# Kernel optimization log

Measured on AMD Instinct MI355X. Metric: run time of the kernel, lower is better.

Reference implementation:

```python
import jax, jax.numpy as jnp
import numpy as np

N = 100000      # nodes
E = 3200000     # edges
F_IN = 128      # input node features
G = 64          # graphs in batch
A = 32          # action_shape


def _fanin_uniform(key, shape):
    v = 1.0 / np.sqrt(shape[0])
    return jax.random.uniform(key, shape, jnp.float32, -v, v)


def setup_inputs() -> dict:
    key = jax.random.key(0)
    ks = jax.random.split(key, 16)
    x = jax.random.normal(ks[0], (N, F_IN), jnp.float32)
    edge_index = jax.random.randint(ks[1], (2, E), 0, N, jnp.int64)
    batch = jnp.sort(jax.random.randint(ks[2], (N,), 0, G, jnp.int64))
    init_w = 0.003
    return {
        "x": x,
        "edge_index": edge_index,
        "batch": batch,
        # GCN weights are [in, out] (old-style PyG GCNConv .weight)
        "W1": _fanin_uniform(ks[3], (F_IN, 16)), "b1": jnp.zeros((16,), jnp.float32),
        "W2": _fanin_uniform(ks[4], (16, 64)),   "b2": jnp.zeros((64,), jnp.float32),
        "W3": _fanin_uniform(ks[5], (64, 32)),   "b3": jnp.zeros((32,), jnp.float32),
        # MLP head (Linear stores [out, in]; we keep [in, out] and matmul directly)
        "Wa": _fanin_uniform(ks[6], (32, 64)),   "ba": jnp.zeros((64,), jnp.float32),
        "Wo": jax.random.uniform(ks[7], (64, A), jnp.float32, -init_w, init_w),
        "bo": jnp.zeros((A,), jnp.float32),
    }


def _gcn_conv(x, W, b, src, dst, dinv):
    # GCNConv: D^{-1/2}(A+I)D^{-1/2} X W + b, symmetric norm with self-loops.
    h = x @ W                                   # [N, out] small GEMM
    coef = dinv[src] * dinv[dst]                # [E]
    msg = h[src] * coef[:, None]                # gather + scale (memory-bound)
    agg = jax.ops.segment_sum(msg, dst, num_segments=N)  # scatter-add
    agg = agg + h * (dinv * dinv)[:, None]      # self-loop contribution
    return agg + b


def reference(x, edge_index, batch, W1, b1, W2, b2, W3, b3, Wa, ba, Wo, bo):
    src, dst = edge_index[0], edge_index[1]
    # degree with self-loops (edge weights = 1)
    deg = jax.ops.segment_sum(jnp.ones((E,), x.dtype), dst, num_segments=N) + 1.0
    dinv = jax.lax.rsqrt(deg)

    h = jax.nn.relu(_gcn_conv(x, W1, b1, src, dst, dinv))   # dropout: eval no-op
    h = jax.nn.relu(_gcn_conv(h, W2, b2, src, dst, dinv))
    h = _gcn_conv(h, W3, b3, src, dst, dinv)                # [N, 32]

    # global_mean_pool over batch ids
    sums = jax.ops.segment_sum(h, batch, num_segments=G)            # [G, 32]
    cnts = jax.ops.segment_sum(jnp.ones((N,), h.dtype), batch, num_segments=G)
    pooled = sums / jnp.maximum(cnts, 1.0)[:, None]

    a = jax.nn.relu(pooled @ Wa + ba)
    return jnp.tanh(a @ Wo + bo)                             # [G, A]
```

## Files before the change

### kernel.cpp

```cpp
#include <hip/hip_runtime.h>
#include <hip/hip_bf16.h>
#include <math.h>


#define THREADS 256
#define TCSR 512
#define BSH 8
#define MAXNB 512
#define CH_E 2048
#define CPT 8

typedef __attribute__((ext_vector_type(8))) short short8;
typedef __attribute__((ext_vector_type(4))) float f32x4;

__device__ inline unsigned short f2bf(float f) {
    unsigned int u = __float_as_uint(f);
    return (unsigned short)((u + 0x7fffu + ((u >> 16) & 1u)) >> 16);
}
__device__ inline unsigned int pk2bf(float a, float b) {
    return (unsigned int)f2bf(a) | ((unsigned int)f2bf(b) << 16);
}
__device__ inline float bflo(unsigned int u) { return __uint_as_float(u << 16); }
__device__ inline float bfhi(unsigned int u) { return __uint_as_float(u & 0xffff0000u); }
__device__ inline void unpk8(const uint4 u, float* f) {
    f[0] = bflo(u.x); f[1] = bfhi(u.x); f[2] = bflo(u.y); f[3] = bfhi(u.y);
    f[4] = bflo(u.z); f[5] = bfhi(u.z); f[6] = bflo(u.w); f[7] = bfhi(u.w);
}

__global__ void k_countA(const int* __restrict__ dst, unsigned short* __restrict__ lp16,
                         int* __restrict__ cnt_mat, int E, int NB, int NCH) {
    __shared__ int hist[MAXNB];
    int t = threadIdx.x, chunk = blockIdx.x;
    for (int h = t; h < NB; h += THREADS) hist[h] = 0;
    __syncthreads();
    int e0 = chunk * CH_E, e1 = min(E, e0 + CH_E);
    for (int e = e0 + t; e < e1; e += THREADS) {
        int h = dst[e] >> BSH;
        int lp = atomicAdd(&hist[h], 1);
        lp16[e] = (unsigned short)lp;
    }
    __syncthreads();
    for (int h = t; h < NB; h += THREADS) cnt_mat[(size_t)h * NCH + chunk] = hist[h];
}

__global__ void k_sumK1(const int* __restrict__ cnt_mat, int* __restrict__ bucket_tot, int NCH) {
    __shared__ int red[THREADS];
    int b = blockIdx.x, t = threadIdx.x;
    int s = 0;
    for (int c = t; c < NCH; c += THREADS) s += cnt_mat[(size_t)b * NCH + c];
    red[t] = s;
    __syncthreads();
    for (int off = THREADS / 2; off > 0; off >>= 1) {
        if (t < off) red[t] += red[t + off];
        __syncthreads();
    }
    if (t == 0) bucket_tot[b] = red[0];
}

__global__ void k_scanK2(const int* __restrict__ bucket_tot, int* __restrict__ bucket_base,
                         int* __restrict__ rowptr, int NB, int E, int N) {
    __shared__ int sh[MAXNB];
    int t = threadIdx.x;
    int v = (t < NB) ? bucket_tot[t] : 0;
    sh[t] = v;
    __syncthreads();
    for (int off = 1; off < MAXNB; off <<= 1) {
        int u = (t >= off) ? sh[t - off] : 0;
        __syncthreads();
        sh[t] += u;
        __syncthreads();
    }
    if (t < NB) bucket_base[t] = sh[t] - v;
    if (t == 0) { bucket_base[NB] = E; rowptr[N] = E; }
}

__global__ void k_scanK3(const int* __restrict__ cnt_mat, const int* __restrict__ bucket_base,
                         int* __restrict__ offs_mat, int NCH) {
    __shared__ int sh[THREADS];
    int b = blockIdx.x, t = threadIdx.x;
    int c0 = t * CPT;
    int v[CPT];
    int s = 0;
#pragma unroll
    for (int k = 0; k < CPT; ++k) {
        int c = c0 + k;
        v[k] = (c < NCH) ? cnt_mat[(size_t)b * NCH + c] : 0;
        s += v[k];
    }
    sh[t] = s;
    __syncthreads();
    for (int off = 1; off < THREADS; off <<= 1) {
        int u = (t >= off) ? sh[t - off] : 0;
        __syncthreads();
        sh[t] += u;
        __syncthreads();
    }
    int run = bucket_base[b] + sh[t] - s;
#pragma unroll
    for (int k = 0; k < CPT; ++k) {
        int c = c0 + k;
        if (c < NCH) { offs_mat[(size_t)b * NCH + c] = run; run += v[k]; }
    }
}

__global__ void k_scatter2(const int* __restrict__ src, const int* __restrict__ dst,
                           const unsigned short* __restrict__ lp16,
                           const int* __restrict__ offs_mat,
                           unsigned int* __restrict__ bedges, int E, int NB, int NCH) {
    __shared__ int offs[MAXNB];
    int t = threadIdx.x, chunk = blockIdx.x;
    for (int h = t; h < NB; h += THREADS) offs[h] = offs_mat[(size_t)h * NCH + chunk];
    __syncthreads();
    int e0 = chunk * CH_E, e1 = min(E, e0 + CH_E);
    for (int e = e0 + t; e < e1; e += THREADS) {
        int d = dst[e];
        int h = d >> BSH;
        int pos = offs[h] + (int)lp16[e];
        bedges[pos] = ((unsigned int)src[e] << BSH) | (unsigned int)(d & ((1 << BSH) - 1));
    }
}

__global__ void k_bucket_csr(const unsigned int* __restrict__ bedges,
                             const int* __restrict__ bucket_base,
                             int* __restrict__ rowptr, float* __restrict__ dinv,
                             int* __restrict__ csr_src, int N) {
    __shared__ int hist[256];
    __shared__ int sc[256];
    __shared__ int cur[256];
    int t = threadIdx.x;
    int b = blockIdx.x;
    int base = bucket_base[b];
    int end = bucket_base[b + 1];
    if (t < 256) hist[t] = 0;
    __syncthreads();
    for (int i = base + t; i < end; i += TCSR)
        atomicAdd(&hist[bedges[i] & 255], 1);
    __syncthreads();
    int c = 0;
    if (t < 256) { c = hist[t]; sc[t] = c; }
    __syncthreads();
    for (int off = 1; off < 256; off <<= 1) {
        int u = (t >= off && t < 256) ? sc[t - off] : 0;
        __syncthreads();
        if (t < 256) sc[t] += u;
        __syncthreads();
    }
    if (t < 256) {
        int excl = sc[t] - c;
        int node = (b << BSH) + t;
        if (node < N) {
            rowptr[node] = base + excl;
            dinv[node] = (float)(1.0 / sqrt((double)(c + 1)));
        }
        cur[t] = excl;
    }
    __syncthreads();
    for (int i = base + t; i < end; i += TCSR) {
        unsigned int u = bedges[i];
        int ln = (int)(u & 255);
        int p = atomicAdd(&cur[ln], 1);
        csr_src[base + p] = (int)(u >> BSH);
    }
}

__global__ __launch_bounds__(256) void k_gemm1(const float* __restrict__ X,
                        const float* __restrict__ W,
                        const float* __restrict__ dinv, unsigned short* __restrict__ H, int N) {
    __shared__ float Wt[16 * 128];
    int t = threadIdx.x;
    for (int i = t; i < 16 * 128; i += THREADS) {
        int j = i >> 7, k = i & 127;
        Wt[i] = W[k * 16 + j];
    }
    __syncthreads();
    int row = blockIdx.x * THREADS + t;
    if (row >= N) return;
    const float4* xr = (const float4*)(X + (size_t)row * 128);
    float acc[16];
#pragma unroll
    for (int j = 0; j < 16; ++j) acc[j] = 0.0f;
#pragma unroll 4
    for (int k4 = 0; k4 < 32; ++k4) {
        float4 xv = xr[k4];
#pragma unroll
        for (int j = 0; j < 16; ++j) {
            const float4 wv = *(const float4*)&Wt[j * 128 + k4 * 4];
            acc[j] += xv.x * wv.x + xv.y * wv.y + xv.z * wv.z + xv.w * wv.w;
        }
    }
    float di = dinv[row];
    uint4 oa, ob;
    oa.x = pk2bf(acc[0] * di, acc[1] * di);
    oa.y = pk2bf(acc[2] * di, acc[3] * di);
    oa.z = pk2bf(acc[4] * di, acc[5] * di);
    oa.w = pk2bf(acc[6] * di, acc[7] * di);
    ob.x = pk2bf(acc[8] * di, acc[9] * di);
    ob.y = pk2bf(acc[10] * di, acc[11] * di);
    ob.z = pk2bf(acc[12] * di, acc[13] * di);
    ob.w = pk2bf(acc[14] * di, acc[15] * di);
    uint4* outr = (uint4*)(H + (size_t)row * 16);
    outr[0] = oa;
    outr[1] = ob;
}

template<int F, int MODE, int S>
__global__ __launch_bounds__(256) void k_pull(
        const int* __restrict__ rowptr, const int* __restrict__ csr_src,
        const float* __restrict__ dinv, const unsigned short* __restrict__ Hb,
        const float* __restrict__ bias, void* __restrict__ outp,
        const int* __restrict__ batch, float* __restrict__ gsums,
        int N, int G) {
    const int LPN = F / 8;
    const int GRP = LPN * S;
    const int NPB = THREADS / GRP;
    int t = threadIdx.x;
    int idx = t % GRP;
    int fl = idx % LPN;
    int s  = idx / LPN;
    int fo = fl * 8;
    int node = blockIdx.x * NPB + t / GRP;

    float acc[8] = {0.f, 0.f, 0.f, 0.f, 0.f, 0.f, 0.f, 0.f};
    if (node < N) {
        int beg = rowptr[node], end = rowptr[node + 1];
        int i = beg + s;
        for (; i + 3 * S < end; i += 4 * S) {
            int s0 = csr_src[i];
            int s1 = csr_src[i + S];
            int s2 = csr_src[i + 2 * S];
            int s3 = csr_src[i + 3 * S];
            uint4 g0 = *(const uint4*)(Hb + (size_t)s0 * F + fo);
            uint4 g1 = *(const uint4*)(Hb + (size_t)s1 * F + fo);
            uint4 g2 = *(const uint4*)(Hb + (size_t)s2 * F + fo);
            uint4 g3 = *(const uint4*)(Hb + (size_t)s3 * F + fo);
            float f0[8], f1[8], f2[8], f3[8];
            unpk8(g0, f0); unpk8(g1, f1); unpk8(g2, f2); unpk8(g3, f3);
#pragma unroll
            for (int j = 0; j < 8; ++j) acc[j] += (f0[j] + f1[j]) + (f2[j] + f3[j]);
        }
        for (; i < end; i += S) {
            int sv = csr_src[i];
            uint4 g = *(const uint4*)(Hb + (size_t)sv * F + fo);
            float f[8];
            unpk8(g, f);
#pragma unroll
            for (int j = 0; j < 8; ++j) acc[j] += f[j];
        }
    }
#pragma unroll
    for (int j = 0; j < 8; ++j) {
        if (S >= 2) acc[j] += __shfl_xor(acc[j], LPN);
        if (S >= 4) acc[j] += __shfl_xor(acc[j], 2 * LPN);
    }

    if constexpr (MODE == 3) {
        __shared__ float lsum[4][32];
        __shared__ int g0s;
        for (int z = t; z < 4 * 32; z += THREADS) ((float*)lsum)[z] = 0.0f;
        if (t == 0) g0s = batch[blockIdx.x * NPB];
        __syncthreads();
        int g0 = g0s;
        if (node < N && s == 0) {
            uint4 gs = *(const uint4*)(Hb + (size_t)node * F + fo);
            float sf[8];
            unpk8(gs, sf);
            float di = dinv[node];
            int g = batch[node];
            int r = g - g0;
            if ((unsigned)r < 4u) {
#pragma unroll
                for (int j = 0; j < 8; ++j)
                    atomicAdd(&lsum[r][fo + j], di * (acc[j] + sf[j]));
            } else {
#pragma unroll
                for (int j = 0; j < 8; ++j)
                    atomicAdd(&gsums[(size_t)g * 32 + fo + j], di * (acc[j] + sf[j]));
            }
        }
        __syncthreads();
        if (t < 128) {
            int r = t >> 5, f = t & 31;
            int g = g0 + r;
            float v = lsum[r][f];
            if (g < G && v != 0.0f) atomicAdd(&gsums[(size_t)g * 32 + f], v);
        }
    } else {
        if (node < N && s == 0) {
            uint4 gs = *(const uint4*)(Hb + (size_t)node * F + fo);
            float sf[8];
            unpk8(gs, sf);
            float di = dinv[node];
            float tv[8];
#pragma unroll
            for (int j = 0; j < 8; ++j) tv[j] = di * (acc[j] + sf[j]);
            if constexpr (MODE == 1) {
                float w[8];
#pragma unroll
                for (int j = 0; j < 8; ++j) w[j] = fmaxf(tv[j] + bias[fo + j], 0.0f) * di;
                uint4 st;
                st.x = pk2bf(w[0], w[1]); st.y = pk2bf(w[2], w[3]);
                st.z = pk2bf(w[4], w[5]); st.w = pk2bf(w[6], w[7]);
                *(uint4*)((unsigned short*)outp + (size_t)node * F + fo) = st;
            } else {
                float* of = (float*)outp + (size_t)node * F + fo;
                float4 o0, o1;
                o0.x = tv[0]; o0.y = tv[1]; o0.z = tv[2]; o0.w = tv[3];
                o1.x = tv[4]; o1.y = tv[5]; o1.z = tv[6]; o1.w = tv[7];
                ((float4*)of)[0] = o0; ((float4*)of)[1] = o1;
            }
        }
    }
}

__global__ __launch_bounds__(256) void k_mlp(const float* __restrict__ P2,
                      const float* __restrict__ W2, const float* __restrict__ b2,
                      const float* __restrict__ W3, const float* __restrict__ dinv,
                      unsigned short* __restrict__ Hb3, int N) {
    __shared__ unsigned int aTd[4][32][17];
    int t = threadIdx.x;
    int w = t >> 6;
    int l = t & 63;
    int g = l >> 4;
    int c = l & 15;
    int node = blockIdx.x * 64 + w * 16 + c;
    bool nv = node < N;
    int cn = nv ? node : 0;

    short8 w2f[4];
#pragma unroll
    for (int mi = 0; mi < 4; ++mi) {
        short8 f = {0, 0, 0, 0, 0, 0, 0, 0};
        if (g < 2) {
            int j = 16 * mi + c;
#pragma unroll
            for (int e = 0; e < 8; ++e)
                f[e] = (short)f2bf(W2[(8 * g + e) * 64 + j]);
        }
        w2f[mi] = f;
    }
    short8 w3f[2][2];
#pragma unroll
    for (int mt = 0; mt < 2; ++mt)
#pragma unroll
        for (int kt = 0; kt < 2; ++kt) {
            short8 f;
#pragma unroll
            for (int e = 0; e < 8; ++e)
                f[e] = (short)f2bf(W3[(32 * kt + 8 * g + e) * 32 + 16 * mt + c]);
            w3f[mt][kt] = f;
        }
    float b2v[16];
#pragma unroll
    for (int mi = 0; mi < 4; ++mi)
#pragma unroll
        for (int r = 0; r < 4; ++r)
            b2v[4 * mi + r] = b2[16 * mi + 4 * g + r];

    short8 pf = {0, 0, 0, 0, 0, 0, 0, 0};
    if (g < 2) {
        const float4* pr = (const float4*)(P2 + (size_t)cn * 16 + 8 * g);
        float4 p0 = pr[0], p1 = pr[1];
        pf[0] = (short)f2bf(p0.x); pf[1] = (short)f2bf(p0.y);
        pf[2] = (short)f2bf(p0.z); pf[3] = (short)f2bf(p0.w);
        pf[4] = (short)f2bf(p1.x); pf[5] = (short)f2bf(p1.y);
        pf[6] = (short)f2bf(p1.z); pf[7] = (short)f2bf(p1.w);
    }

    f32x4 zero = {0.f, 0.f, 0.f, 0.f};
    f32x4 acc1[4];
#pragma unroll
    for (int mi = 0; mi < 4; ++mi)
        acc1[mi] = __builtin_amdgcn_mfma_f32_16x16x32_bf16(w2f[mi], pf, zero, 0, 0, 0);

#pragma unroll
    for (int mi = 0; mi < 4; ++mi) {
        float a0 = fmaxf(acc1[mi][0] + b2v[4 * mi + 0], 0.f);
        float a1 = fmaxf(acc1[mi][1] + b2v[4 * mi + 1], 0.f);
        float a2 = fmaxf(acc1[mi][2] + b2v[4 * mi + 2], 0.f);
        float a3 = fmaxf(acc1[mi][3] + b2v[4 * mi + 3], 0.f);
        aTd[w][8 * mi + 2 * g][c]     = pk2bf(a0, a1);
        aTd[w][8 * mi + 2 * g + 1][c] = pk2bf(a2, a3);
    }
    __syncthreads();

    short8 bfr[2];
#pragma unroll
    for (int kt = 0; kt < 2; ++kt) {
        short8 f;
#pragma unroll
        for (int i = 0; i < 4; ++i) {
            unsigned int d = aTd[w][16 * kt + 4 * g + i][c];
            f[2 * i]     = (short)(d & 0xffffu);
            f[2 * i + 1] = (short)(d >> 16);
        }
        bfr[kt] = f;
    }

    f32x4 acc2[2] = {{0.f, 0.f, 0.f, 0.f}, {0.f, 0.f, 0.f, 0.f}};
#pragma unroll
    for (int mt = 0; mt < 2; ++mt)
#pragma unroll
        for (int kt = 0; kt < 2; ++kt)
            acc2[mt] = __builtin_amdgcn_mfma_f32_16x16x32_bf16(w3f[mt][kt], bfr[kt], acc2[mt], 0, 0, 0);

    if (nv) {
        float di = dinv[node];
        unsigned short* o = Hb3 + (size_t)node * 32;
#pragma unroll
        for (int mt = 0; mt < 2; ++mt) {
            *(unsigned int*)(o + 16 * mt + 4 * g)     = pk2bf(acc2[mt][0] * di, acc2[mt][1] * di);
            *(unsigned int*)(o + 16 * mt + 4 * g + 2) = pk2bf(acc2[mt][2] * di, acc2[mt][3] * di);
        }
    }
}

__global__ void k_zero_f(float* p, int n) {
    int i = blockIdx.x * blockDim.x + threadIdx.x;
    if (i < n) p[i] = 0.0f;
}

__global__ void k_head(const float* __restrict__ sums, const int* __restrict__ batch, int N,
                       const float* __restrict__ b3,
                       const float* __restrict__ Wa, const float* __restrict__ ba,
                       const float* __restrict__ Wo, const float* __restrict__ bo,
                       float* __restrict__ out) {
    int g = blockIdx.x;
    int j = threadIdx.x;
    int lo = 0, hi = N;
    while (lo < hi) { int m = (lo + hi) >> 1; if (batch[m] < g) lo = m + 1; else hi = m; }
    int start = lo;
    lo = start; hi = N;
    while (lo < hi) { int m = (lo + hi) >> 1; if (batch[m] < g + 1) lo = m + 1; else hi = m; }
    int cnt = lo - start;
    float inv = 1.0f / (float)(cnt > 0 ? cnt : 1);

    __shared__ float p[32];
    __shared__ float a[64];
    if (j < 32) p[j] = sums[g * 32 + j] * inv + b3[j];
    __syncthreads();
    float acc = ba[j];
#pragma unroll
    for (int k = 0; k < 32; ++k) acc += p[k] * Wa[k * 64 + j];
    a[j] = fmaxf(acc, 0.0f);
    __syncthreads();
    if (j < 32) {
        float acc2 = bo[j];
#pragma unroll
        for (int k = 0; k < 64; ++k) acc2 += a[k] * Wo[k * 32 + j];
        out[g * 32 + j] = tanhf(acc2);
    }
}

static inline int cdiv(long long a, int b) { return (int)((a + b - 1) / b); }
static inline size_t align256(size_t x) { return (x + 255) & ~(size_t)255; }

extern "C" void kernel_launch(void* const* d_in, const int* in_sizes, int n_in,
                              void* d_out, int out_size, void* d_ws, size_t ws_size,
                              hipStream_t stream) {
    const float* x     = (const float*)d_in[0];
    const int*   edge  = (const int*)d_in[1];
    const int*   batch = (const int*)d_in[2];
    const float* W1 = (const float*)d_in[3];  const float* b1 = (const float*)d_in[4];
    const float* W2 = (const float*)d_in[5];  const float* b2 = (const float*)d_in[6];
    const float* W3 = (const float*)d_in[7];  const float* b3 = (const float*)d_in[8];
    const float* Wa = (const float*)d_in[9];  const float* ba = (const float*)d_in[10];
    const float* Wo = (const float*)d_in[11]; const float* bo = (const float*)d_in[12];

    const int E = in_sizes[1] / 2;
    const int N = in_sizes[2];
    const int G = 64;
    const int NB = cdiv(N, 1 << BSH);
    const int NCH = cdiv(E, CH_E);

    const int* srcp = edge;
    const int* dstp = edge + E;

    char* base = (char*)d_ws;
    size_t off = 0;
    float* dinv   = (float*)(base + off); off = align256(off + sizeof(float) * N);
    unsigned short* lp16 = (unsigned short*)(base + off); off = align256(off + sizeof(short) * E);
    int* cnt_mat  = (int*)(base + off); off = align256(off + sizeof(int) * (size_t)NB * NCH);
    int* offs_mat = (int*)(base + off); off = align256(off + sizeof(int) * (size_t)NB * NCH);
    int* btot     = (int*)(base + off); off = align256(off + sizeof(int) * (NB + 1));
    int* bbase    = (int*)(base + off); off = align256(off + sizeof(int) * (NB + 1));
    unsigned int* bedges = (unsigned int*)(base + off); off = align256(off + sizeof(int) * E);
    int* rowptr   = (int*)(base + off); off = align256(off + sizeof(int) * (N + 1));
    int* csr_src  = (int*)(base + off); off = align256(off + sizeof(int) * E);
    unsigned short* Hb1 = (unsigned short*)(base + off); off = align256(off + sizeof(short) * (size_t)N * 16);
    unsigned short* Hb2 = (unsigned short*)(base + off); off = align256(off + sizeof(short) * (size_t)N * 16);
    float* P2     = (float*)(base + off); off = align256(off + sizeof(float) * (size_t)N * 16);
    unsigned short* Hb3 = (unsigned short*)(base + off); off = align256(off + sizeof(short) * (size_t)N * 32);
    float* sums   = (float*)(base + off); off = align256(off + sizeof(float) * G * 32);

    k_countA<<<NCH, THREADS, 0, stream>>>(dstp, lp16, cnt_mat, E, NB, NCH);
    k_sumK1<<<NB, THREADS, 0, stream>>>(cnt_mat, btot, NCH);
    k_scanK2<<<1, MAXNB, 0, stream>>>(btot, bbase, rowptr, NB, E, N);
    k_scanK3<<<NB, THREADS, 0, stream>>>(cnt_mat, bbase, offs_mat, NCH);
    k_scatter2<<<NCH, THREADS, 0, stream>>>(srcp, dstp, lp16, offs_mat, bedges, E, NB, NCH);

    k_bucket_csr<<<NB, TCSR, 0, stream>>>(bedges, bbase, rowptr, dinv, csr_src, N);

    k_gemm1<<<cdiv(N, THREADS), THREADS, 0, stream>>>(x, W1, dinv, Hb1, N);
    k_pull<16, 1, 4><<<cdiv(N, 32), THREADS, 0, stream>>>(rowptr, csr_src, dinv, Hb1, b1, Hb2,
                                                          nullptr, nullptr, N, G);

    k_pull<16, 2, 4><<<cdiv(N, 32), THREADS, 0, stream>>>(rowptr, csr_src, dinv, Hb2, nullptr, P2,
                                                          nullptr, nullptr, N, G);

    k_mlp<<<cdiv(N, 64), THREADS, 0, stream>>>(P2, W2, b2, W3, dinv, Hb3, N);

    k_zero_f<<<cdiv(G * 32, THREADS), THREADS, 0, stream>>>(sums, G * 32);
    k_pull<32, 3, 2><<<cdiv(N, 32), THREADS, 0, stream>>>(rowptr, csr_src, dinv, Hb3, nullptr,
                                                          nullptr, batch, sums, N, G);

    k_head<<<G, 64, 0, stream>>>(sums, batch, N, b3, Wa, ba, Wo, bo, (float*)d_out);
}
```

Before: 310.5 us.

## Split layer-3 features into two 16-wide halves and pull each half separately

The layer-3 hidden state is stored as two separate 16-feature bf16 arrays instead of one 32-wide array, and the final aggregation-plus-pooling runs as a new kernel where each block handles one half for 64 nodes. Each half-array is 3.2 MB, so the random neighbour gathers touch a smaller footprint that fits better in cache. The cost is reading the CSR indices twice and issuing more global atomics into the pooled sums. The edge chunk size for CSR construction is also doubled.

```diff
diff --git a/kernel.cpp b/kernel.cpp
--- a/kernel.cpp
+++ b/kernel.cpp
@@ -7,7 +7,7 @@
 #define TCSR 512
 #define BSH 8
 #define MAXNB 512
-#define CH_E 2048
+#define CH_E 4096
 #define CPT 8
 
 typedef __attribute__((ext_vector_type(8))) short short8;
@@ -207,9 +207,7 @@
 __global__ __launch_bounds__(256) void k_pull(
         const int* __restrict__ rowptr, const int* __restrict__ csr_src,
         const float* __restrict__ dinv, const unsigned short* __restrict__ Hb,
-        const float* __restrict__ bias, void* __restrict__ outp,
-        const int* __restrict__ batch, float* __restrict__ gsums,
-        int N, int G) {
+        const float* __restrict__ bias, void* __restrict__ outp, int N) {
     const int LPN = F / 8;
     const int GRP = LPN * S;
     const int NPB = THREADS / GRP;
@@ -253,69 +251,118 @@
         if (S >= 4) acc[j] += __shfl_xor(acc[j], 2 * LPN);
     }
 
-    if constexpr (MODE == 3) {
-        __shared__ float lsum[4][32];
-        __shared__ int g0s;
-        for (int z = t; z < 4 * 32; z += THREADS) ((float*)lsum)[z] = 0.0f;
-        if (t == 0) g0s = batch[blockIdx.x * NPB];
-        __syncthreads();
-        int g0 = g0s;
-        if (node < N && s == 0) {
-            uint4 gs = *(const uint4*)(Hb + (size_t)node * F + fo);
-            float sf[8];
-            unpk8(gs, sf);
-            float di = dinv[node];
-            int g = batch[node];
-            int r = g - g0;
-            if ((unsigned)r < 4u) {
-#pragma unroll
-                for (int j = 0; j < 8; ++j)
-                    atomicAdd(&lsum[r][fo + j], di * (acc[j] + sf[j]));
-            } else {
-#pragma unroll
-                for (int j = 0; j < 8; ++j)
-                    atomicAdd(&gsums[(size_t)g * 32 + fo + j], di * (acc[j] + sf[j]));
-            }
-        }
-        __syncthreads();
-        if (t < 128) {
-            int r = t >> 5, f = t & 31;
-            int g = g0 + r;
-            float v = lsum[r][f];
-            if (g < G && v != 0.0f) atomicAdd(&gsums[(size_t)g * 32 + f], v);
-        }
-    } else {
-        if (node < N && s == 0) {
-            uint4 gs = *(const uint4*)(Hb + (size_t)node * F + fo);
-            float sf[8];
-            unpk8(gs, sf);
-            float di = dinv[node];
-            float tv[8];
-#pragma unroll
-            for (int j = 0; j < 8; ++j) tv[j] = di * (acc[j] + sf[j]);
-            if constexpr (MODE == 1) {
-                float w[8];
-#pragma unroll
-                for (int j = 0; j < 8; ++j) w[j] = fmaxf(tv[j] + bias[fo + j], 0.0f) * di;
-                uint4 st;
-                st.x = pk2bf(w[0], w[1]); st.y = pk2bf(w[2], w[3]);
-                st.z = pk2bf(w[4], w[5]); st.w = pk2bf(w[6], w[7]);
-                *(uint4*)((unsigned short*)outp + (size_t)node * F + fo) = st;
-            } else {
-                float* of = (float*)outp + (size_t)node * F + fo;
-                float4 o0, o1;
-                o0.x = tv[0]; o0.y = tv[1]; o0.z = tv[2]; o0.w = tv[3];
-                o1.x = tv[4]; o1.y = tv[5]; o1.z = tv[6]; o1.w = tv[7];
-                ((float4*)of)[0] = o0; ((float4*)of)[1] = o1;
-            }
-        }
+    if (node < N && s == 0) {
+        uint4 gs = *(const uint4*)(Hb + (size_t)node * F + fo);
+        float sf[8];
+        unpk8(gs, sf);
+        float di = dinv[node];
+        float tv[8];
+#pragma unroll
+        for (int j = 0; j < 8; ++j) tv[j] = di * (acc[j] + sf[j]);
+        if constexpr (MODE == 1) {
+            float w[8];
+#pragma unroll
+            for (int j = 0; j < 8; ++j) w[j] = fmaxf(tv[j] + bias[fo + j], 0.0f) * di;
+            uint4 st;
+            st.x = pk2bf(w[0], w[1]); st.y = pk2bf(w[2], w[3]);
+            st.z = pk2bf(w[4], w[5]); st.w = pk2bf(w[6], w[7]);
+            *(uint4*)((unsigned short*)outp + (size_t)node * F + fo) = st;
+        } else {
+            float* of = (float*)outp + (size_t)node * F + fo;
+            float4 o0, o1;
+            o0.x = tv[0]; o0.y = tv[1]; o0.z = tv[2]; o0.w = tv[3];
+            o1.x = tv[4]; o1.y = tv[5]; o1.z = tv[6]; o1.w = tv[7];
+            ((float4*)of)[0] = o0; ((float4*)of)[1] = o1;
+        }
+    }
+}
+
+__global__ __launch_bounds__(256) void k_pull3(
+        const int* __restrict__ rowptr, const int* __restrict__ csr_src,
+        const float* __restrict__ dinv, const unsigned short* __restrict__ HbA,
+        const unsigned short* __restrict__ HbB, const int* __restrict__ batch,
+        float* __restrict__ gsums, int N, int G, int nwg) {
+    __shared__ float lsum[4][16];
+    __shared__ int g0s;
+    int bid = blockIdx.x;
+    int q = bid >> 3, r = bid & 7;
+    int half = r >> 2;
+    int idx = q * 4 + (r & 3);
+    if (idx >= nwg) return;
+    const unsigned short* Hb = half ? HbB : HbA;
+    int t = threadIdx.x;
+    int l4 = t & 3;
+    int fl = l4 & 1;
+    int s  = l4 >> 1;
+    int fo = fl * 8;
+    int node = idx * 64 + (t >> 2);
+
+    if (t < 64) ((float*)lsum)[t] = 0.0f;
+    if (t == 0) g0s = batch[idx * 64];
+    __syncthreads();
+
+    float acc[8] = {0.f, 0.f, 0.f, 0.f, 0.f, 0.f, 0.f, 0.f};
+    if (node < N) {
+        int beg = rowptr[node], end = rowptr[node + 1];
+        int i = beg + s;
+        for (; i + 6 < end; i += 8) {
+            int s0 = csr_src[i];
+            int s1 = csr_src[i + 2];
+            int s2 = csr_src[i + 4];
+            int s3 = csr_src[i + 6];
+            uint4 g0 = *(const uint4*)(Hb + (size_t)s0 * 16 + fo);
+            uint4 g1 = *(const uint4*)(Hb + (size_t)s1 * 16 + fo);
+            uint4 g2 = *(const uint4*)(Hb + (size_t)s2 * 16 + fo);
+            uint4 g3 = *(const uint4*)(Hb + (size_t)s3 * 16 + fo);
+            float f0[8], f1[8], f2[8], f3[8];
+            unpk8(g0, f0); unpk8(g1, f1); unpk8(g2, f2); unpk8(g3, f3);
+#pragma unroll
+            for (int j = 0; j < 8; ++j) acc[j] += (f0[j] + f1[j]) + (f2[j] + f3[j]);
+        }
+        for (; i < end; i += 2) {
+            int sv = csr_src[i];
+            uint4 g = *(const uint4*)(Hb + (size_t)sv * 16 + fo);
+            float f[8];
+            unpk8(g, f);
+#pragma unroll
+            for (int j = 0; j < 8; ++j) acc[j] += f[j];
+        }
+    }
+#pragma unroll
+    for (int j = 0; j < 8; ++j) acc[j] += __shfl_xor(acc[j], 2);
+
+    int g0 = g0s;
+    if (node < N && s == 0) {
+        uint4 gs = *(const uint4*)(Hb + (size_t)node * 16 + fo);
+        float sf[8];
+        unpk8(gs, sf);
+        float di = dinv[node];
+        int g = batch[node];
+        int rr = g - g0;
+        if ((unsigned)rr < 4u) {
+#pragma unroll
+            for (int j = 0; j < 8; ++j)
+                atomicAdd(&lsum[rr][fo + j], di * (acc[j] + sf[j]));
+        } else {
+#pragma unroll
+            for (int j = 0; j < 8; ++j)
+                atomicAdd(&gsums[(size_t)g * 32 + half * 16 + fo + j], di * (acc[j] + sf[j]));
+        }
+    }
+    __syncthreads();
+    if (t < 64) {
+        int rr = t >> 4, f = t & 15;
+        int g = g0 + rr;
+        float v = lsum[rr][f];
+        if (g < G && v != 0.0f) atomicAdd(&gsums[(size_t)g * 32 + half * 16 + f], v);
     }
 }
 
 __global__ __launch_bounds__(256) void k_mlp(const float* __restrict__ P2,
                       const float* __restrict__ W2, const float* __restrict__ b2,
                       const float* __restrict__ W3, const float* __restrict__ dinv,
-                      unsigned short* __restrict__ Hb3, int N) {
+                      unsigned short* __restrict__ Hb3a, unsigned short* __restrict__ Hb3b,
+                      int N) {
     __shared__ unsigned int aTd[4][32][17];
     int t = threadIdx.x;
     int w = t >> 6;
@@ -405,12 +452,12 @@
 
     if (nv) {
         float di = dinv[node];
-        unsigned short* o = Hb3 + (size_t)node * 32;
-#pragma unroll
-        for (int mt = 0; mt < 2; ++mt) {
-            *(unsigned int*)(o + 16 * mt + 4 * g)     = pk2bf(acc2[mt][0] * di, acc2[mt][1] * di);
-            *(unsigned int*)(o + 16 * mt + 4 * g + 2) = pk2bf(acc2[mt][2] * di, acc2[mt][3] * di);
-        }
+        unsigned short* oA = Hb3a + (size_t)node * 16;
+        unsigned short* oB = Hb3b + (size_t)node * 16;
+        *(unsigned int*)(oA + 4 * g)     = pk2bf(acc2[0][0] * di, acc2[0][1] * di);
+        *(unsigned int*)(oA + 4 * g + 2) = pk2bf(acc2[0][2] * di, acc2[0][3] * di);
+        *(unsigned int*)(oB + 4 * g)     = pk2bf(acc2[1][0] * di, acc2[1][1] * di);
+        *(unsigned int*)(oB + 4 * g + 2) = pk2bf(acc2[1][2] * di, acc2[1][3] * di);
     }
 }
 
@@ -489,7 +536,8 @@
     unsigned short* Hb1 = (unsigned short*)(base + off); off = align256(off + sizeof(short) * (size_t)N * 16);
     unsigned short* Hb2 = (unsigned short*)(base + off); off = align256(off + sizeof(short) * (size_t)N * 16);
     float* P2     = (float*)(base + off); off = align256(off + sizeof(float) * (size_t)N * 16);
-    unsigned short* Hb3 = (unsigned short*)(base + off); off = align256(off + sizeof(short) * (size_t)N * 32);
+    unsigned short* Hb3a = (unsigned short*)(base + off); off = align256(off + sizeof(short) * (size_t)N * 16);
+    unsigned short* Hb3b = (unsigned short*)(base + off); off = align256(off + sizeof(short) * (size_t)N * 16);
     float* sums   = (float*)(base + off); off = align256(off + sizeof(float) * G * 32);
 
     k_countA<<<NCH, THREADS, 0, stream>>>(dstp, lp16, cnt_mat, E, NB, NCH);
@@ -501,17 +549,18 @@
     k_bucket_csr<<<NB, TCSR, 0, stream>>>(bedges, bbase, rowptr, dinv, csr_src, N);
 
     k_gemm1<<<cdiv(N, THREADS), THREADS, 0, stream>>>(x, W1, dinv, Hb1, N);
-    k_pull<16, 1, 4><<<cdiv(N, 32), THREADS, 0, stream>>>(rowptr, csr_src, dinv, Hb1, b1, Hb2,
-                                                          nullptr, nullptr, N, G);
-
-    k_pull<16, 2, 4><<<cdiv(N, 32), THREADS, 0, stream>>>(rowptr, csr_src, dinv, Hb2, nullptr, P2,
-                                                          nullptr, nullptr, N, G);
-
-    k_mlp<<<cdiv(N, 64), THREADS, 0, stream>>>(P2, W2, b2, W3, dinv, Hb3, N);
+    k_pull<16, 1, 4><<<cdiv(N, 32), THREADS, 0, stream>>>(rowptr, csr_src, dinv, Hb1, b1, Hb2, N);
+
+    k_pull<16, 2, 4><<<cdiv(N, 32), THREADS, 0, stream>>>(rowptr, csr_src, dinv, Hb2, nullptr, P2, N);
+
+    k_mlp<<<cdiv(N, 64), THREADS, 0, stream>>>(P2, W2, b2, W3, dinv, Hb3a, Hb3b, N);
 
     k_zero_f<<<cdiv(G * 32, THREADS), THREADS, 0, stream>>>(sums, G * 32);
-    k_pull<32, 3, 2><<<cdiv(N, 32), THREADS, 0, stream>>>(rowptr, csr_src, dinv, Hb3, nullptr,
-                                                          nullptr, batch, sums, N, G);
+    {
+        const int nwg3 = cdiv(N, 64);
+        k_pull3<<<8 * cdiv(nwg3, 4), THREADS, 0, stream>>>(rowptr, csr_src, dinv, Hb3a, Hb3b,
+                                                           batch, sums, N, G, nwg3);
+    }
 
     k_head<<<G, 64, 0, stream>>>(sums, batch, N, b3, Wa, ba, Wo, bo, (float*)d_out);
 }
```

Result: slower. 319.4 us (+2.9%).

## Replace final GCN pull layer with source-bucketed push into per-graph pooled sums

Applied to the files above, without the earlier changes.

The last GCN layer plus mean pool is rewritten. Each edge now contributes dinv[dst]*H3[src] straight to the graph sum of its destination, using a second bucketed edge list sorted by source, built alongside the destination one. Per-block shared-memory partials are reduced into the global graph sums. This avoids a full per-node aggregation and write of the last layer, and lets each block read H3 rows from a narrow source range for locality. The cost is a second counting and scatter pass over all edges, plus many shared atomics in the push kernel. The edge chunk size is also doubled.

```diff
diff --git a/kernel.cpp b/kernel.cpp
--- a/kernel.cpp
+++ b/kernel.cpp
@@ -7,8 +7,9 @@
 #define TCSR 512
 #define BSH 8
 #define MAXNB 512
-#define CH_E 2048
+#define CH_E 4096
 #define CPT 8
+#define PSPLIT 4
 
 typedef __attribute__((ext_vector_type(8))) short short8;
 typedef __attribute__((ext_vector_type(4))) float f32x4;
@@ -27,20 +28,27 @@
     f[4] = bflo(u.z); f[5] = bfhi(u.z); f[6] = bflo(u.w); f[7] = bfhi(u.w);
 }
 
-__global__ void k_countA(const int* __restrict__ dst, unsigned short* __restrict__ lp16,
-                         int* __restrict__ cnt_mat, int E, int NB, int NCH) {
-    __shared__ int hist[MAXNB];
+__global__ void k_countA2(const int* __restrict__ src, const int* __restrict__ dst,
+                          unsigned short* __restrict__ lpd, unsigned short* __restrict__ lps,
+                          int* __restrict__ cnt_d, int* __restrict__ cnt_s,
+                          int E, int NB, int NCH) {
+    __shared__ int hd[MAXNB];
+    __shared__ int hs[MAXNB];
     int t = threadIdx.x, chunk = blockIdx.x;
-    for (int h = t; h < NB; h += THREADS) hist[h] = 0;
+    for (int h = t; h < NB; h += THREADS) { hd[h] = 0; hs[h] = 0; }
     __syncthreads();
     int e0 = chunk * CH_E, e1 = min(E, e0 + CH_E);
     for (int e = e0 + t; e < e1; e += THREADS) {
-        int h = dst[e] >> BSH;
-        int lp = atomicAdd(&hist[h], 1);
-        lp16[e] = (unsigned short)lp;
-    }
-    __syncthreads();
-    for (int h = t; h < NB; h += THREADS) cnt_mat[(size_t)h * NCH + chunk] = hist[h];
+        int hD = dst[e] >> BSH;
+        lpd[e] = (unsigned short)atomicAdd(&hd[hD], 1);
+        int hS = src[e] >> BSH;
+        lps[e] = (unsigned short)atomicAdd(&hs[hS], 1);
+    }
+    __syncthreads();
+    for (int h = t; h < NB; h += THREADS) {
+        cnt_d[(size_t)h * NCH + chunk] = hd[h];
+        cnt_s[(size_t)h * NCH + chunk] = hs[h];
+    }
 }
 
 __global__ void k_sumK1(const int* __restrict__ cnt_mat, int* __restrict__ bucket_tot, int NCH) {
@@ -74,8 +82,8 @@
     if (t == 0) { bucket_base[NB] = E; rowptr[N] = E; }
 }
 
-__global__ void k_scanK3(const int* __restrict__ cnt_mat, const int* __restrict__ bucket_base,
-                         int* __restrict__ offs_mat, int NCH) {
+__global__ void k_scanK3(int* __restrict__ cnt_mat, const int* __restrict__ bucket_base,
+                         int NCH) {
     __shared__ int sh[THREADS];
     int b = blockIdx.x, t = threadIdx.x;
     int c0 = t * CPT;
@@ -99,30 +107,40 @@
 #pragma unroll
     for (int k = 0; k < CPT; ++k) {
         int c = c0 + k;
-        if (c < NCH) { offs_mat[(size_t)b * NCH + c] = run; run += v[k]; }
-    }
-}
-
-__global__ void k_scatter2(const int* __restrict__ src, const int* __restrict__ dst,
-                           const unsigned short* __restrict__ lp16,
-                           const int* __restrict__ offs_mat,
-                           unsigned int* __restrict__ bedges, int E, int NB, int NCH) {
-    __shared__ int offs[MAXNB];
+        if (c < NCH) { cnt_mat[(size_t)b * NCH + c] = run; run += v[k]; }
+    }
+}
+
+__global__ void k_scatter2x2(const int* __restrict__ src, const int* __restrict__ dst,
+                             const unsigned short* __restrict__ lpd,
+                             const unsigned short* __restrict__ lps,
+                             const int* __restrict__ offs_d, const int* __restrict__ offs_s,
+                             unsigned int* __restrict__ bedges_d,
+                             unsigned int* __restrict__ bedges_s,
+                             int E, int NB, int NCH) {
+    __shared__ int od[MAXNB];
+    __shared__ int osrc[MAXNB];
     int t = threadIdx.x, chunk = blockIdx.x;
-    for (int h = t; h < NB; h += THREADS) offs[h] = offs_mat[(size_t)h * NCH + chunk];
+    for (int h = t; h < NB; h += THREADS) {
+        od[h] = offs_d[(size_t)h * NCH + chunk];
+        osrc[h] = offs_s[(size_t)h * NCH + chunk];
+    }
     __syncthreads();
     int e0 = chunk * CH_E, e1 = min(E, e0 + CH_E);
     for (int e = e0 + t; e < e1; e += THREADS) {
-        int d = dst[e];
-        int h = d >> BSH;
-        int pos = offs[h] + (int)lp16[e];
-        bedges[pos] = ((unsigned int)src[e] << BSH) | (unsigned int)(d & ((1 << BSH) - 1));
+        int s = src[e], d = dst[e];
+        int posd = od[d >> BSH] + (int)lpd[e];
+        bedges_d[posd] = ((unsigned int)s << BSH) | (unsigned int)(d & ((1 << BSH) - 1));
+        int poss = osrc[s >> BSH] + (int)lps[e];
+        bedges_s[poss] = ((unsigned int)d << BSH) | (unsigned int)(s & ((1 << BSH) - 1));
     }
 }
 
 __global__ void k_bucket_csr(const unsigned int* __restrict__ bedges,
                              const int* __restrict__ bucket_base,
+                             const int* __restrict__ batch,
                              int* __restrict__ rowptr, float* __restrict__ dinv,
+                             float2* __restrict__ bd,
                              int* __restrict__ csr_src, int N) {
     __shared__ int hist[256];
     __shared__ int sc[256];
@@ -150,7 +168,9 @@
         int node = (b << BSH) + t;
         if (node < N) {
             rowptr[node] = base + excl;
-            dinv[node] = (float)(1.0 / sqrt((double)(c + 1)));
+            float dv = (float)(1.0 / sqrt((double)(c + 1)));
+            dinv[node] = dv;
+            bd[node] = make_float2(dv, __int_as_float(batch[node]));
         }
         cur[t] = excl;
     }
@@ -207,9 +227,7 @@
 __global__ __launch_bounds__(256) void k_pull(
         const int* __restrict__ rowptr, const int* __restrict__ csr_src,
         const float* __restrict__ dinv, const unsigned short* __restrict__ Hb,
-        const float* __restrict__ bias, void* __restrict__ outp,
-        const int* __restrict__ batch, float* __restrict__ gsums,
-        int N, int G) {
+        const float* __restrict__ bias, void* __restrict__ outp, int N) {
     const int LPN = F / 8;
     const int GRP = LPN * S;
     const int NPB = THREADS / GRP;
@@ -253,61 +271,28 @@
         if (S >= 4) acc[j] += __shfl_xor(acc[j], 2 * LPN);
     }
 
-    if constexpr (MODE == 3) {
-        __shared__ float lsum[4][32];
-        __shared__ int g0s;
-        for (int z = t; z < 4 * 32; z += THREADS) ((float*)lsum)[z] = 0.0f;
-        if (t == 0) g0s = batch[blockIdx.x * NPB];
-        __syncthreads();
-        int g0 = g0s;
-        if (node < N && s == 0) {
-            uint4 gs = *(const uint4*)(Hb + (size_t)node * F + fo);
-            float sf[8];
-            unpk8(gs, sf);
-            float di = dinv[node];
-            int g = batch[node];
-            int r = g - g0;
-            if ((unsigned)r < 4u) {
-#pragma unroll
-                for (int j = 0; j < 8; ++j)
-                    atomicAdd(&lsum[r][fo + j], di * (acc[j] + sf[j]));
-            } else {
-#pragma unroll
-                for (int j = 0; j < 8; ++j)
-                    atomicAdd(&gsums[(size_t)g * 32 + fo + j], di * (acc[j] + sf[j]));
-            }
-        }
-        __syncthreads();
-        if (t < 128) {
-            int r = t >> 5, f = t & 31;
-            int g = g0 + r;
-            float v = lsum[r][f];
-            if (g < G && v != 0.0f) atomicAdd(&gsums[(size_t)g * 32 + f], v);
-        }
-    } else {
-        if (node < N && s == 0) {
-            uint4 gs = *(const uint4*)(Hb + (size_t)node * F + fo);
-            float sf[8];
-            unpk8(gs, sf);
-            float di = dinv[node];
-            float tv[8];
-#pragma unroll
-            for (int j = 0; j < 8; ++j) tv[j] = di * (acc[j] + sf[j]);
-            if constexpr (MODE == 1) {
-                float w[8];
-#pragma unroll
-                for (int j = 0; j < 8; ++j) w[j] = fmaxf(tv[j] + bias[fo + j], 0.0f) * di;
-                uint4 st;
-                st.x = pk2bf(w[0], w[1]); st.y = pk2bf(w[2], w[3]);
-                st.z = pk2bf(w[4], w[5]); st.w = pk2bf(w[6], w[7]);
-                *(uint4*)((unsigned short*)outp + (size_t)node * F + fo) = st;
-            } else {
-                float* of = (float*)outp + (size_t)node * F + fo;
-                float4 o0, o1;
-                o0.x = tv[0]; o0.y = tv[1]; o0.z = tv[2]; o0.w = tv[3];
-                o1.x = tv[4]; o1.y = tv[5]; o1.z = tv[6]; o1.w = tv[7];
-                ((float4*)of)[0] = o0; ((float4*)of)[1] = o1;
-            }
+    if (node < N && s == 0) {
+        uint4 gs = *(const uint4*)(Hb + (size_t)node * F + fo);
+        float sf[8];
+        unpk8(gs, sf);
+        float di = dinv[node];
+        float tv[8];
+#pragma unroll
+        for (int j = 0; j < 8; ++j) tv[j] = di * (acc[j] + sf[j]);
+        if constexpr (MODE == 1) {
+            float w[8];
+#pragma unroll
+            for (int j = 0; j < 8; ++j) w[j] = fmaxf(tv[j] + bias[fo + j], 0.0f) * di;
+            uint4 st;
+            st.x = pk2bf(w[0], w[1]); st.y = pk2bf(w[2], w[3]);
+            st.z = pk2bf(w[4], w[5]); st.w = pk2bf(w[6], w[7]);
+            *(uint4*)((unsigned short*)outp + (size_t)node * F + fo) = st;
+        } else {
+            float* of = (float*)outp + (size_t)node * F + fo;
+            float4 o0, o1;
+            o0.x = tv[0]; o0.y = tv[1]; o0.z = tv[2]; o0.w = tv[3];
+            o1.x = tv[4]; o1.y = tv[5]; o1.z = tv[6]; o1.w = tv[7];
+            ((float4*)of)[0] = o0; ((float4*)of)[1] = o1;
         }
     }
 }
@@ -412,6 +397,66 @@
             *(unsigned int*)(o + 16 * mt + 4 * g + 2) = pk2bf(acc2[mt][2] * di, acc2[mt][3] * di);
         }
     }
+}
+
+__global__ __launch_bounds__(256) void k_push(
+        const unsigned int* __restrict__ bsrc, const int* __restrict__ bbase_s,
+        const float2* __restrict__ bd, const unsigned short* __restrict__ Hb3,
+        float* __restrict__ partials, int N) {
+    __shared__ float acc[64][33];
+    int t = threadIdx.x;
+    int bid = blockIdx.x;
+    int b = bid >> 2, p = bid & 3;
+    for (int i = t; i < 64 * 33; i += THREADS) ((float*)acc)[i] = 0.0f;
+    __syncthreads();
+    int e0 = bbase_s[b], e1 = bbase_s[b + 1];
+    int len = e1 - e0;
+    int s0 = e0 + (int)(((long long)len * p) >> 2);
+    int s1 = e0 + (int)(((long long)len * (p + 1)) >> 2);
+    int q = t & 3, fo = q * 8;
+    for (int i = s0 + (t >> 2); i < s1; i += 64) {
+        unsigned int w = bsrc[i];
+        int srcn = (b << BSH) | (int)(w & 255u);
+        int dstn = (int)(w >> BSH);
+        float2 v = bd[dstn];
+        float di = v.x;
+        int g = __float_as_int(v.y);
+        uint4 gr = *(const uint4*)(Hb3 + (size_t)srcn * 32 + fo);
+        float f[8];
+        unpk8(gr, f);
+#pragma unroll
+        for (int j = 0; j < 8; ++j) atomicAdd(&acc[g][fo + j], di * f[j]);
+    }
+    if (p == 0) {
+        int n0 = b << BSH;
+        int n1 = min(N, n0 + 256);
+        for (int n = n0 + (t >> 2); n < n1; n += 64) {
+            float2 v = bd[n];
+            float di = v.x;
+            int g = __float_as_int(v.y);
+            uint4 gr = *(const uint4*)(Hb3 + (size_t)n * 32 + fo);
+            float f[8];
+            unpk8(gr, f);
+#pragma unroll
+            for (int j = 0; j < 8; ++j) atomicAdd(&acc[g][fo + j], di * f[j]);
+        }
+    }
+    __syncthreads();
+    float* out = partials + (size_t)bid * 2048;
+    for (int i = t; i < 2048; i += THREADS) out[i] = acc[i >> 5][i & 31];
+}
+
+__global__ void k_reduce(const float* __restrict__ partials, float* __restrict__ sums,
+                         int NBLK) {
+    int blk = blockIdx.x;
+    int t = threadIdx.x;
+    int fid = (blk & 7) * 256 + t;
+    int r = blk >> 3;
+    int b0 = (int)(((long long)NBLK * r) >> 2);
+    int b1 = (int)(((long long)NBLK * (r + 1)) >> 2);
+    float s = 0.0f;
+    for (int b = b0; b < b1; ++b) s += partials[(size_t)b * 2048 + fid];
+    atomicAdd(&sums[fid], s);
 }
 
 __global__ void k_zero_f(float* p, int n) {
@@ -478,40 +523,48 @@
     char* base = (char*)d_ws;
     size_t off = 0;
     float* dinv   = (float*)(base + off); off = align256(off + sizeof(float) * N);
-    unsigned short* lp16 = (unsigned short*)(base + off); off = align256(off + sizeof(short) * E);
-    int* cnt_mat  = (int*)(base + off); off = align256(off + sizeof(int) * (size_t)NB * NCH);
-    int* offs_mat = (int*)(base + off); off = align256(off + sizeof(int) * (size_t)NB * NCH);
-    int* btot     = (int*)(base + off); off = align256(off + sizeof(int) * (NB + 1));
-    int* bbase    = (int*)(base + off); off = align256(off + sizeof(int) * (NB + 1));
-    unsigned int* bedges = (unsigned int*)(base + off); off = align256(off + sizeof(int) * E);
+    float2* bd    = (float2*)(base + off); off = align256(off + sizeof(float2) * N);
+    unsigned short* lpd = (unsigned short*)(base + off); off = align256(off + sizeof(short) * E);
+    unsigned short* lps = (unsigned short*)(base + off); off = align256(off + sizeof(short) * E);
+    int* cnt_d    = (int*)(base + off); off = align256(off + sizeof(int) * (size_t)NB * NCH);
+    int* cnt_s    = (int*)(base + off); off = align256(off + sizeof(int) * (size_t)NB * NCH);
+    int* btot_d   = (int*)(base + off); off = align256(off + sizeof(int) * (NB + 1));
+    int* bbase_d  = (int*)(base + off); off = align256(off + sizeof(int) * (NB + 1));
+    int* btot_s   = (int*)(base + off); off = align256(off + sizeof(int) * (NB + 1));
+    int* bbase_s  = (int*)(base + off); off = align256(off + sizeof(int) * (NB + 1));
+    unsigned int* bedges_d = (unsigned int*)(base + off); off = align256(off + sizeof(int) * E);
+    unsigned int* bedges_s = (unsigned int*)(base + off); off = align256(off + sizeof(int) * E);
     int* rowptr   = (int*)(base + off); off = align256(off + sizeof(int) * (N + 1));
     int* csr_src  = (int*)(base + off); off = align256(off + sizeof(int) * E);
     unsigned short* Hb1 = (unsigned short*)(base + off); off = align256(off + sizeof(short) * (size_t)N * 16);
     unsigned short* Hb2 = (unsigned short*)(base + off); off = align256(off + sizeof(short) * (size_t)N * 16);
     float* P2     = (float*)(base + off); off = align256(off + sizeof(float) * (size_t)N * 16);
     unsigned short* Hb3 = (unsigned short*)(base + off); off = align256(off + sizeof(short) * (size_t)N * 32);
+    float* partials = (float*)(base + off); off = align256(off + sizeof(float) * (size_t)(PSPLIT * NB) * 2048);
     float* sums   = (float*)(base + off); off = align256(off + sizeof(float) * G * 32);
 
-    k_countA<<<NCH, THREADS, 0, stream>>>(dstp, lp16, cnt_mat, E, NB, NCH);
-    k_sumK1<<<NB, THREADS, 0, stream>>>(cnt_mat, btot, NCH);
-    k_scanK2<<<1, MAXNB, 0, stream>>>(btot, bbase, rowptr, NB, E, N);
-    k_scanK3<<<NB, THREADS, 0, stream>>>(cnt_mat, bbase, offs_mat, NCH);
-    k_scatter2<<<NCH, THREADS, 0, stream>>>(srcp, dstp, lp16, offs_mat, bedges, E, NB, NCH);
-
-    k_bucket_csr<<<NB, TCSR, 0, stream>>>(bedges, bbase, rowptr, dinv, csr_src, N);
+    k_countA2<<<NCH, THREADS, 0, stream>>>(srcp, dstp, lpd, lps, cnt_d, cnt_s, E, NB, NCH);
+    k_sumK1<<<NB, THREADS, 0, stream>>>(cnt_d, btot_d, NCH);
+    k_sumK1<<<NB, THREADS, 0, stream>>>(cnt_s, btot_s, NCH);
+    k_scanK2<<<1, MAXNB, 0, stream>>>(btot_d, bbase_d, rowptr, NB, E, N);
+    k_scanK2<<<1, MAXNB, 0, stream>>>(btot_s, bbase_s, rowptr, NB, E, N);
+    k_scanK3<<<NB, THREADS, 0, stream>>>(cnt_d, bbase_d, NCH);
+    k_scanK3<<<NB, THREADS, 0, stream>>>(cnt_s, bbase_s, NCH);
+    k_scatter2x2<<<NCH, THREADS, 0, stream>>>(srcp, dstp, lpd, lps, cnt_d, cnt_s,
+                                              bedges_d, bedges_s, E, NB, NCH);
+
+    k_bucket_csr<<<NB, TCSR, 0, stream>>>(bedges_d, bbase_d, batch, rowptr, dinv, bd, csr_src, N);
 
     k_gemm1<<<cdiv(N, THREADS), THREADS, 0, stream>>>(x, W1, dinv, Hb1, N);
-    k_pull<16, 1, 4><<<cdiv(N, 32), THREADS, 0, stream>>>(rowptr, csr_src, dinv, Hb1, b1, Hb2,
-                                                          nullptr, nullptr, N, G);
-
-    k_pull<16, 2, 4><<<cdiv(N, 32), THREADS, 0, stream>>>(rowptr, csr_src, dinv, Hb2, nullptr, P2,
-                                                          nullptr, nullptr, N, G);
+    k_pull<16, 1, 4><<<cdiv(N, 32), THREADS, 0, stream>>>(rowptr, csr_src, dinv, Hb1, b1, Hb2, N);
+
+    k_pull<16, 2, 4><<<cdiv(N, 32), THREADS, 0, stream>>>(rowptr, csr_src, dinv, Hb2, nullptr, P2, N);
 
     k_mlp<<<cdiv(N, 64), THREADS, 0, stream>>>(P2, W2, b2, W3, dinv, Hb3, N);
 
     k_zero_f<<<cdiv(G * 32, THREADS), THREADS, 0, stream>>>(sums, G * 32);
-    k_pull<32, 3, 2><<<cdiv(N, 32), THREADS, 0, stream>>>(rowptr, csr_src, dinv, Hb3, nullptr,
-                                                          nullptr, batch, sums, N, G);
+    k_push<<<PSPLIT * NB, THREADS, 0, stream>>>(bedges_s, bbase_s, bd, Hb3, partials, N);
+    k_reduce<<<32, THREADS, 0, stream>>>(partials, sums, PSPLIT * NB);
 
     k_head<<<G, 64, 0, stream>>>(sums, batch, N, b3, Wa, ba, Wo, bo, (float*)d_out);
 }
```

Result: slower. 1.068 ms (+243.9%).
